# Performance work log

Measured on AMD Instinct MI355X. Metric: run time of the kernel, lower is better.

The kernel has to match this reference:

```python
import jax, jax.numpy as jnp
import numpy as np

D_MODEL, N_HEADS, D_HEAD = 1024, 16, 64
BATCH, SEQ = 4, 2048


def setup_inputs() -> dict:
    key = jax.random.key(0)
    ks = jax.random.split(key, 10)
    s = 1.0 / np.sqrt(D_MODEL)
    x = jax.random.normal(ks[0], (BATCH, SEQ, D_MODEL), dtype=jnp.float32)
    attention_mask = jax.random.randint(ks[1], (BATCH, SEQ), 0, 2).astype(jnp.bool_)
    # guarantee at least one attended key per batch row (avoid all -inf softmax)
    attention_mask = attention_mask.at[:, 0].set(True)
    def lin(k):
        kw, kb = jax.random.split(k)
        W = jax.random.uniform(kw, (D_MODEL, D_MODEL), jnp.float32, -s, s)
        b = jax.random.uniform(kb, (D_MODEL,), jnp.float32, -s, s)
        return W, b
    Wq, bq = lin(ks[2]); Wk, bk = lin(ks[3]); Wv, bv = lin(ks[4]); Wo, bo = lin(ks[5])
    return {"x": x, "attention_mask": attention_mask,
            "Wq": Wq, "bq": bq, "Wk": Wk, "bk": bk,
            "Wv": Wv, "bv": bv, "Wo": Wo, "bo": bo}


def reference(x, attention_mask, Wq, bq, Wk, bk, Wv, bv, Wo, bo):
    B, S, _ = x.shape
    def proj(W, b):  # [B,S,d_model] -> [B,S,H,Dh]
        return (x @ W + b).reshape(B, S, N_HEADS, D_HEAD)
    q = proj(Wq, bq)
    k = proj(Wk, bk)
    v = proj(Wv, bv)
    scores = jnp.einsum('bqhd,bkhd->bhqk', q, k)  # [B,H,S,S]
    add_mask = jnp.where(attention_mask, 0.0, jnp.inf)[:, None, None, :]
    # faithful order: subtract mask, THEN scale (inf survives division)
    probs = jax.nn.softmax((scores - add_mask) / jnp.sqrt(jnp.float32(D_HEAD)), axis=-1)
    attn = jnp.einsum('bhqk,bkhd->bqhd', probs, v).reshape(B, S, N_HEADS * D_HEAD)
    return attn @ Wo + bo
```

## Files before the change

kernel.cpp:

```cpp
#include <hip/hip_runtime.h>
#include <hip/hip_bf16.h>
#include <math.h>

#define BATCH 4
#define SEQ   2048
#define DM    1024
#define NH    16
#define DH    64
#define MROWS (BATCH * SEQ)

typedef unsigned short ushort_t;
typedef unsigned int   uint_t;
typedef __attribute__((ext_vector_type(8))) short  short8;
typedef __attribute__((ext_vector_type(4))) float  float4v;

#define QSCALE 0.1803368801111244f

__device__ __forceinline__ ushort_t f2bf(float v) {
    uint_t u = __float_as_uint(v);
    u += 0x7FFFu + ((u >> 16) & 1u);
    return (ushort_t)(u >> 16);
}
__device__ __forceinline__ float bf2f(ushort_t h) {
    return __uint_as_float(((uint_t)h) << 16);
}
__device__ __forceinline__ void gload_lds16(const ushort_t* g, ushort_t* lds) {
    __builtin_amdgcn_global_load_lds(
        (const __attribute__((address_space(1))) void*)g,
        (__attribute__((address_space(3))) void*)lds, 16, 0, 0);
}

__global__ __launch_bounds__(256) void conv_x(
    const float* __restrict__ src, ushort_t* __restrict__ dst, int n4)
{
    int i = blockIdx.x * 256 + threadIdx.x;
#pragma unroll
    for (int k = 0; k < 4; k++, i += 524288) {
        float4 v = ((const float4*)src)[i];
        ((ushort4*)dst)[i] = make_ushort4(f2bf(v.x), f2bf(v.y), f2bf(v.z), f2bf(v.w));
    }
}

__global__ __launch_bounds__(256) void convT_w4(
    const float* __restrict__ W0, const float* __restrict__ W1,
    const float* __restrict__ W2, const float* __restrict__ W3,
    ushort_t* __restrict__ fused, ushort_t* __restrict__ woh,
    ushort_t* __restrict__ wol)
{
    __shared__ float sT[64][65];
    const int z = blockIdx.z;
    const float* W = (z == 0) ? W0 : (z == 1) ? W1 : (z == 2) ? W2 : W3;
    ushort_t* ht = (z < 3) ? fused + (size_t)z * 1024 * 1024 : woh;
    const int n0 = blockIdx.x * 64, k0 = blockIdx.y * 64;
    const int t = threadIdx.x;
#pragma unroll
    for (int i = 0; i < 16; i++) {
        int idx = t + i * 256, r = idx >> 6, c = idx & 63;
        sT[r][c] = W[(size_t)(k0 + r) * 1024 + n0 + c];
    }
    __syncthreads();
#pragma unroll
    for (int i = 0; i < 16; i++) {
        int idx = t + i * 256, r = idx >> 6, c = idx & 63;
        float v = sT[c][r];
        ushort_t h = f2bf(v);
        ht[(size_t)(n0 + r) * 1024 + k0 + c] = h;
        if (z == 3) wol[(size_t)(n0 + r) * 1024 + k0 + c] = f2bf(v - bf2f(h));
    }
}

#define BAR()   asm volatile("s_barrier" ::: "memory")
#define LGKM0() asm volatile("s_waitcnt lgkmcnt(0)" ::: "memory")
#define VMW6()  asm volatile("s_waitcnt vmcnt(6)" ::: "memory")

#define STAGE_A(BO, KT) do {                                                 \
    const ushort_t* _s = prowA + (size_t)((KT) & 15) * 64;                   \
    gload_lds16(_s,         &smem[(BO) + dstw]);                             \
    gload_lds16(_s + 65536, &smem[(BO) + 4096 + dstw]);                      \
  } while (0)

#define STAGE_B(BO, KT) do {                                                 \
    const ushort_t* _s = prowB + (size_t)((KT) & 15) * 64;                   \
    gload_lds16(_s,          &smem[(BO) + 8192  + dstw]);                    \
    gload_lds16(_s + 65536,  &smem[(BO) + 12288 + dstw]);                    \
    gload_lds16(_s + 131072, &smem[(BO) + 16384 + dstw]);                    \
    gload_lds16(_s + 196608, &smem[(BO) + 20480 + dstw]);                    \
  } while (0)

#define LOAD_AV(BO) do {                                                     \
    _Pragma("unroll")                                                        \
    for (int mf = 0; mf < 4; mf++) {                                         \
      av[mf][0] = *(const short8*)&smem[(BO) + aAm + mf * 1024 + aA0];       \
      av[mf][1] = *(const short8*)&smem[(BO) + aAm + mf * 1024 + aA1];       \
    }                                                                        \
  } while (0)

#define LOAD_BV(BO, NQ) do {                                                 \
    _Pragma("unroll")                                                        \
    for (int nf = 0; nf < 2; nf++) {                                         \
      bvf[nf][0] = *(const short8*)&smem[(BO) + 8192 + aBn + (NQ) * 2048 +   \
                                         nf * 1024 + aA0];                   \
      bvf[nf][1] = *(const short8*)&smem[(BO) + 8192 + aBn + (NQ) * 2048 +   \
                                         nf * 1024 + aA1];                   \
    }                                                                        \
  } while (0)

#define MFMA_H(NQ) do {                                                      \
    __builtin_amdgcn_s_setprio(1);                                           \
    _Pragma("unroll")                                                        \
    for (int kk = 0; kk < 2; kk++)                                           \
      _Pragma("unroll")                                                      \
      for (int nf = 0; nf < 2; nf++)                                         \
        _Pragma("unroll")                                                    \
        for (int mf = 0; mf < 4; mf++)                                       \
          acc[mf][(NQ) * 2 + nf] =                                           \
              __builtin_amdgcn_mfma_f32_16x16x32_bf16(                       \
                  av[mf][kk], bvf[nf][kk], acc[mf][(NQ) * 2 + nf], 0, 0, 0); \
    __builtin_amdgcn_s_setprio(0);                                           \
  } while (0)

__global__ __launch_bounds__(512, 2) void gemm_qkv(
    const ushort_t* __restrict__ A, const ushort_t* __restrict__ Bt,
    const float* __restrict__ bq, const float* __restrict__ bk,
    const float* __restrict__ bv, const int* __restrict__ mask,
    ushort_t* __restrict__ Qh, ushort_t* __restrict__ Kh,
    ushort_t* __restrict__ Vt)
{
    __shared__ __align__(16) ushort_t smem[73728];
    const int t = threadIdx.x, lane = t & 63, w = t >> 6;

    int bid = blockIdx.y * 12 + blockIdx.x;
    bid = (bid & 7) * 96 + (bid >> 3);
    const int n0 = (bid % 12) * 256, m0 = (bid / 12) * 128;

    const int wm = w >> 2, wn = w & 3;
    const int lq = lane >> 4, lc = lane & 15;
    const int gl = (lane & 7) ^ ((lane >> 3) & 7);
    const int sect = n0 >> 10;
    const float* bsel = (sect == 0) ? bq : (sect == 1) ? bk : bv;
    const float scl = (sect == 0) ? QSCALE : 1.0f;

    const ushort_t* prowA = A  + (size_t)(m0 + w * 8 + (lane >> 3)) * 1024 + gl * 8;
    const ushort_t* prowB = Bt + (size_t)(n0 + w * 8 + (lane >> 3)) * 1024 + gl * 8;
    const int dstw = w * 512;

    const int aA0 = lc * 64 + ((lq ^ (lc & 7)) * 8);
    const int aA1 = lc * 64 + (((4 + lq) ^ (lc & 7)) * 8);
    const int aAm = wm * 4096;
    const int aBn = wn * 4096;

    float4v acc[4][4];
#pragma unroll
    for (int i = 0; i < 4; i++)
#pragma unroll
        for (int j = 0; j < 4; j++) acc[i][j] = (float4v)(0.0f);

    short8 av[4][2], bvf[2][2];

    STAGE_A(0, 0); STAGE_B(0, 0); STAGE_A(24576, 1); STAGE_B(24576, 1);
    VMW6();
    BAR();

    int bc = 0, bs = 49152;
    for (int kt = 0; kt < 16; kt++) {
        LOAD_AV(bc); LOAD_BV(bc, 0); STAGE_A(bs, kt + 2);
        BAR(); LGKM0(); MFMA_H(0); BAR();
        LOAD_BV(bc, 1); STAGE_B(bs, kt + 2);
        BAR(); LGKM0(); MFMA_H(1); VMW6(); BAR();
        bc = (bc == 49152) ? 0 : bc + 24576;
        bs = (bs == 49152) ? 0 : bs + 24576;
    }

#pragma unroll
    for (int nf = 0; nf < 4; nf++) {
        const int nn = (n0 + wn * 64 + nf * 16 + lc) & 1023;
        const float bvv = bsel[nn];
        const int h = nn >> 6, d = nn & 63;
#pragma unroll
        for (int mf = 0; mf < 4; mf++) {
            const int mbase = m0 + wm * 64 + mf * 16 + lq * 4;
            const int b = mbase >> 11, s0 = mbase & 2047;
            int mk[4] = {1, 1, 1, 1};
            if (sect != 0) {
                const int4 m4 = *(const int4*)&mask[b * 2048 + s0];
                mk[0] = m4.x; mk[1] = m4.y; mk[2] = m4.z; mk[3] = m4.w;
            }
            if (sect == 2) {
                ushort_t hh[4];
#pragma unroll
                for (int r = 0; r < 4; r++)
                    hh[r] = mk[r] ? f2bf(acc[mf][nf][r] + bvv) : (ushort_t)0;
                *(ushort4*)&Vt[((size_t)(b * 16 + h) * 64 + d) * 2048 + s0] =
                    make_ushort4(hh[0], hh[1], hh[2], hh[3]);
            } else {
                ushort_t* dst = (sect == 0) ? Qh : Kh;
#pragma unroll
                for (int r = 0; r < 4; r++)
                    dst[((size_t)(b * 16 + h) * 2048 + s0 + r) * 64 + d] =
                        mk[r] ? f2bf((acc[mf][nf][r] + bvv) * scl) : (ushort_t)0;
            }
        }
    }
}

#undef STAGE_A
#undef STAGE_B
#undef LOAD_AV
#undef LOAD_BV
#undef MFMA_H

#define S3_STAGE3A(BO, KT) do {                                              \
    const size_t _k = (size_t)((KT) & 31) * 32;                              \
    gload_lds16(pAh + _k, &smem[(BO) + toff]);                               \
    gload_lds16(pAl + _k, &smem[(BO) + 4096 + toff]);                        \
    gload_lds16(pBh + _k, &smem[(BO) + 8192 + toff]);                        \
  } while (0)

#define S3_STAGE3B(BO, KT) do {                                              \
    const size_t _k = (size_t)((KT) & 31) * 32;                              \
    gload_lds16(pBh + 131072 + _k, &smem[(BO) + 12288 + toff]);              \
    gload_lds16(pBl + _k,          &smem[(BO) + 16384 + toff]);              \
    gload_lds16(pBl + 131072 + _k, &smem[(BO) + 20480 + toff]);              \
  } while (0)

#define S3_MFMA(NQ) do {                                                     \
    __builtin_amdgcn_s_setprio(1);                                           \
    _Pragma("unroll")                                                        \
    for (int nf = 0; nf < 2; nf++)                                           \
      _Pragma("unroll")                                                      \
      for (int mf = 0; mf < 4; mf++) {                                       \
        float4v* _a = &acc[mf][(NQ) * 2 + nf];                               \
        *_a = __builtin_amdgcn_mfma_f32_16x16x32_bf16(ah[mf], bh[nf], *_a, 0, 0, 0); \
        *_a = __builtin_amdgcn_mfma_f32_16x16x32_bf16(al[mf], bh[nf], *_a, 0, 0, 0); \
        *_a = __builtin_amdgcn_mfma_f32_16x16x32_bf16(ah[mf], bl[nf], *_a, 0, 0, 0); \
      }                                                                      \
    __builtin_amdgcn_s_setprio(0);                                           \
  } while (0)

__global__ __launch_bounds__(512, 2) void gemm_split3(
    const ushort_t* __restrict__ Ah, const ushort_t* __restrict__ Al,
    const ushort_t* __restrict__ Bh, const ushort_t* __restrict__ Bl,
    const float* __restrict__ bias, float* __restrict__ out)
{
    __shared__ __align__(16) ushort_t smem[73728];
    const int t = threadIdx.x, lane = t & 63, w = t >> 6;

    int bid = blockIdx.y * 4 + blockIdx.x;
    bid = (bid & 7) * 32 + (bid >> 3);
    const int n0 = (bid % 4) * 256, m0 = (bid / 4) * 128;

    const int wm = w >> 2, wn = w & 3;
    const int lq = lane >> 4, lc = lane & 15;

    const int prow = t >> 2;
    const int pc = (t & 3) ^ (prow & 3);
    const size_t offA = (size_t)(m0 + prow) * 1024 + pc * 8;
    const size_t offB = (size_t)(n0 + prow) * 1024 + pc * 8;
    const ushort_t* pAh = Ah + offA;
    const ushort_t* pAl = Al + offA;
    const ushort_t* pBh = Bh + offB;
    const ushort_t* pBl = Bl + offB;
    const int toff = t * 8;

    const int aR = lc * 32 + ((lq ^ (lc & 3)) * 8);
    const int aAm = wm * 2048;
    const int aBn = wn * 2048;

    float4v acc[4][4];
#pragma unroll
    for (int i = 0; i < 4; i++)
#pragma unroll
        for (int j = 0; j < 4; j++) acc[i][j] = (float4v)(0.0f);

    short8 ah[4], al[4], bh[2], bl[2];

    S3_STAGE3A(0, 0);     S3_STAGE3B(0, 0);
    S3_STAGE3A(24576, 1); S3_STAGE3B(24576, 1);
    VMW6();
    BAR();

    int bc = 0, bs = 49152;
    for (int kt = 0; kt < 32; kt++) {
#pragma unroll
        for (int mf = 0; mf < 4; mf++) {
            ah[mf] = *(const short8*)&smem[bc + aAm + mf * 512 + aR];
            al[mf] = *(const short8*)&smem[bc + 4096 + aAm + mf * 512 + aR];
        }
#pragma unroll
        for (int nf = 0; nf < 2; nf++) {
            bh[nf] = *(const short8*)&smem[bc + 8192 + aBn + nf * 512 + aR];
            bl[nf] = *(const short8*)&smem[bc + 16384 + aBn + nf * 512 + aR];
        }
        S3_STAGE3A(bs, kt + 2);
        BAR(); LGKM0(); S3_MFMA(0); BAR();

#pragma unroll
        for (int nf = 0; nf < 2; nf++) {
            bh[nf] = *(const short8*)&smem[bc + 8192 + aBn + 1024 + nf * 512 + aR];
            bl[nf] = *(const short8*)&smem[bc + 16384 + aBn + 1024 + nf * 512 + aR];
        }
        S3_STAGE3B(bs, kt + 2);
        BAR(); LGKM0(); S3_MFMA(1); VMW6(); BAR();

        bc = (bc == 49152) ? 0 : bc + 24576;
        bs = (bs == 49152) ? 0 : bs + 24576;
    }

#pragma unroll
    for (int nf = 0; nf < 4; nf++) {
        const int n = n0 + wn * 64 + nf * 16 + lc;
        const float bvv = bias[n];
#pragma unroll
        for (int mf = 0; mf < 4; mf++)
#pragma unroll
            for (int r = 0; r < 4; r++) {
                const int m = m0 + wm * 64 + mf * 16 + lq * 4 + r;
                out[(size_t)m * 1024 + n] = acc[mf][nf][r] + bvv;
            }
    }
}

#undef S3_STAGE3A
#undef S3_STAGE3B
#undef S3_MFMA
#undef BAR
#undef LGKM0
#undef VMW6

#define FBAR()  asm volatile("s_barrier" ::: "memory")
#define FVMW4() asm volatile("s_waitcnt vmcnt(4)" ::: "memory")

__global__ __launch_bounds__(512, 2) void flash_mfma(
    const ushort_t* __restrict__ Q, const ushort_t* __restrict__ K,
    const ushort_t* __restrict__ Vt, const int* __restrict__ mask,
    ushort_t* __restrict__ Oh, ushort_t* __restrict__ Ol)
{
    __shared__ __align__(16) ushort_t smem[57344];
    const int t = threadIdx.x, lane = t & 63, w = t >> 6;

    const int i = blockIdx.y * 4 + blockIdx.x;
    const int bh = (i & 7) + ((i >> 5) << 3);
    const int q0 = ((i >> 3) & 3) * 512;
    const int b = bh >> 4, h = bh & 15;

    const int lq = lane >> 4, lc = lane & 15, lc7 = lc & 7;
    const int wq = w * 64;

    const int4 ma = ((const int4*)(mask + b * SEQ))[t];

    const int trow = lane >> 3;
    const int gl = (lane & 7) ^ (trow & 7);
    const ushort_t* qsrc = Q + ((size_t)bh * SEQ + q0 + wq + trow) * 64 + gl * 8;
#pragma unroll
    for (int j = 0; j < 8; j++)
        gload_lds16(qsrc + j * 512, &smem[w * 4096 + j * 512 + lane * 8]);

    const int strow = t >> 3;
    const int sgl = (t & 7) ^ (strow & 7);
    const ushort_t* kbase = K  + ((size_t)bh * SEQ + strow) * 64 + sgl * 8;
    const ushort_t* vbase = Vt + ((size_t)bh * 64 + strow) * SEQ + sgl * 8;
    gload_lds16(kbase,        &smem[32768 + t * 8]);
    gload_lds16(vbase,        &smem[45056 + t * 8]);
    gload_lds16(kbase + 4096, &smem[32768 + 4096 + t * 8]);
    gload_lds16(vbase + 64,   &smem[45056 + 4096 + t * 8]);

    int cnt = (ma.x == 0) + (ma.y == 0) + (ma.z == 0) + (ma.w == 0);
#pragma unroll
    for (int off = 1; off < 64; off <<= 1) cnt += __shfl_xor(cnt, off);
    if (lane == 0) ((float*)&smem[40960])[w] = (float)cnt;

    FBAR();

    const float* cs = (const float*)&smem[40960];
    const float nmaskf = cs[0] + cs[1] + cs[2] + cs[3] +
                         cs[4] + cs[5] + cs[6] + cs[7];

    FVMW4();
    short8 aq[4][2];
#pragma unroll
    for (int mt = 0; mt < 4; mt++)
#pragma unroll
        for (int kk = 0; kk < 2; kk++) {
            const int r = mt * 16 + lc;
            aq[mt][kk] = *(const short8*)&smem[w * 4096 + r * 64 +
                                               (((kk * 4 + lq) ^ (r & 7)) * 8)];
        }
    FBAR();

    int aK[2], aPw[4];
#pragma unroll
    for (int kk = 0; kk < 2; kk++)
        aK[kk] = lc * 64 + (((kk * 4 + lq) ^ lc7) * 8);
#pragma unroll
    for (int kt4 = 0; kt4 < 4; kt4++)
        aPw[kt4] = lc * 64 + (((kt4 * 2 + (lq >> 1)) ^ lc7) * 8) + (lq & 1) * 4;

    float4v O[4][4];
    float ladd[4];
#pragma unroll
    for (int mt = 0; mt < 4; mt++) {
#pragma unroll
        for (int nt = 0; nt < 4; nt++) O[mt][nt] = (float4v)(0.0f);
        ladd[mt] = 0.0f;
    }

    int cb = 0, sb = 2;
    for (int kt = 0; kt < 32; kt++) {
        const int kn = (kt + 2) & 31;
        gload_lds16(kbase + kn * 4096, &smem[32768 + sb * 4096 + t * 8]);
        gload_lds16(vbase + kn * 64,   &smem[45056 + sb * 4096 + t * 8]);
        FVMW4();
        FBAR();

        const int kb = 32768 + cb * 4096;
        const int vb = 45056 + cb * 4096;
        const int pb = w * 4096;

#pragma unroll
        for (int kt4 = 0; kt4 < 4; kt4++) {
            float4v sc[4];
#pragma unroll
            for (int mt = 0; mt < 4; mt++) sc[mt] = (float4v)(0.0f);
#pragma unroll
            for (int kk = 0; kk < 2; kk++) {
                const short8 ak = *(const short8*)&smem[kb + kt4 * 1024 + aK[kk]];
#pragma unroll
                for (int mt = 0; mt < 4; mt++)
                    sc[mt] = __builtin_amdgcn_mfma_f32_16x16x32_bf16(ak, aq[mt][kk], sc[mt], 0, 0, 0);
            }
#pragma unroll
            for (int mt = 0; mt < 4; mt++) {
                const float p0 = __builtin_amdgcn_exp2f(sc[mt][0]);
                const float p1 = __builtin_amdgcn_exp2f(sc[mt][1]);
                const float p2 = __builtin_amdgcn_exp2f(sc[mt][2]);
                const float p3 = __builtin_amdgcn_exp2f(sc[mt][3]);
                __hip_bfloat162 pk01 = __float22bfloat162_rn(make_float2(p0, p1));
                __hip_bfloat162 pk23 = __float22bfloat162_rn(make_float2(p2, p3));
                const uint_t u01 = *(const uint_t*)&pk01;
                const uint_t u23 = *(const uint_t*)&pk23;
                ladd[mt] += __uint_as_float(u01 << 16) + __uint_as_float(u01 & 0xffff0000u)
                          + __uint_as_float(u23 << 16) + __uint_as_float(u23 & 0xffff0000u);
                *(uint2*)&smem[pb + mt * 1024 + aPw[kt4]] = make_uint2(u01, u23);
            }
        }

#pragma unroll
        for (int kk = 0; kk < 2; kk++) {
            short8 ap[4];
#pragma unroll
            for (int mt = 0; mt < 4; mt++)
                ap[mt] = *(const short8*)&smem[pb + mt * 1024 + aK[kk]];
            __builtin_amdgcn_s_setprio(1);
#pragma unroll
            for (int nt = 0; nt < 4; nt++) {
                const short8 bv = *(const short8*)&smem[vb + nt * 1024 + aK[kk]];
#pragma unroll
                for (int mt = 0; mt < 4; mt++)
                    O[mt][nt] = __builtin_amdgcn_mfma_f32_16x16x32_bf16(ap[mt], bv, O[mt][nt], 0, 0, 0);
            }
            __builtin_amdgcn_s_setprio(0);
        }
        FBAR();

        cb = (cb == 2) ? 0 : cb + 1;
        sb = (sb == 2) ? 0 : sb + 1;
    }

    float lred[4];
#pragma unroll
    for (int mt = 0; mt < 4; mt++) {
        float v = ladd[mt];
        v += __shfl_xor(v, 16);
        v += __shfl_xor(v, 32);
        lred[mt] = v;
    }
    if (lq == 0) {
#pragma unroll
        for (int mt = 0; mt < 4; mt++)
            ((float*)smem)[w * 2048 + mt * 16 + lc] = lred[mt];
    }
    __syncthreads();

#pragma unroll
    for (int mt = 0; mt < 4; mt++) {
#pragma unroll
        for (int r = 0; r < 4; r++) {
            const float lsum =
                ((const float*)smem)[w * 2048 + mt * 16 + lq * 4 + r] - nmaskf;
            const float inv = 1.0f / lsum;
            const int srow = q0 + wq + mt * 16 + lq * 4 + r;
#pragma unroll
            for (int nt = 0; nt < 4; nt++) {
                const float v = O[mt][nt][r] * inv;
                const ushort_t hh = f2bf(v);
                const size_t idx = ((size_t)(b * SEQ + srow)) * 1024 + h * 64 + nt * 16 + lc;
                Oh[idx] = hh;
                Ol[idx] = f2bf(v - bf2f(hh));
            }
        }
    }
}

#undef FBAR
#undef FVMW4

extern "C" void kernel_launch(void* const* d_in, const int* in_sizes, int n_in,
                              void* d_out, int out_size, void* d_ws, size_t ws_size,
                              hipStream_t stream) {
    const float* x    = (const float*)d_in[0];
    const int*   mask = (const int*)d_in[1];
    const float* Wq   = (const float*)d_in[2];
    const float* bq   = (const float*)d_in[3];
    const float* Wk   = (const float*)d_in[4];
    const float* bk   = (const float*)d_in[5];
    const float* Wv   = (const float*)d_in[6];
    const float* bv   = (const float*)d_in[7];
    const float* Wo   = (const float*)d_in[8];
    const float* bo   = (const float*)d_in[9];
    float* out = (float*)d_out;

    ushort_t* p = (ushort_t*)d_ws;
    const size_t PLANE  = (size_t)MROWS * DM;
    const size_t WPLANE = (size_t)DM * DM;
    ushort_t* xh  = p;  p += PLANE;
    ushort_t* wf  = p;  p += 3 * WPLANE;
    ushort_t* woh = p;  p += WPLANE;
    ushort_t* wol = p;  p += WPLANE;
    ushort_t* Qh  = p;  p += PLANE;
    ushort_t* Kh  = p;  p += PLANE;
    ushort_t* Vth = p;  p += PLANE;
    ushort_t* Ath = p;  p += PLANE;
    ushort_t* Atl = p;  p += PLANE;

    dim3 blk(256);
    hipLaunchKernelGGL(conv_x, dim3(2048), blk, 0, stream, x, xh, 2097152);
    hipLaunchKernelGGL(convT_w4, dim3(16, 16, 4), blk, 0, stream,
                       Wq, Wk, Wv, Wo, wf, woh, wol);
    hipLaunchKernelGGL(gemm_qkv, dim3(12, 64), dim3(512), 0, stream,
                       xh, wf, bq, bk, bv, mask, Qh, Kh, Vth);
    hipLaunchKernelGGL(flash_mfma, dim3(4, 64), dim3(512), 0, stream,
                       Qh, Kh, Vth, mask, Ath, Atl);
    hipLaunchKernelGGL(gemm_split3, dim3(4, 64), dim3(512), 0, stream,
                       Ath, Atl, woh, wol, bo, out);
}
```

Measured before the change: 323.8 us.

## Shrink flash blocks to 256 threads, double-buffer K/V, compute row sums via MFMA

The flash attention kernel moves from 512-thread blocks covering 512 queries to 256-thread blocks covering 256 queries. Shared memory drops from 112 KB to 64 KB, and the triple-buffered K/V ring becomes a two-stage buffer that waits on vmcnt(0) at the end of each iteration. The softmax denominator is now accumulated by an extra MFMA against a ones vector instead of scalar bf16 unpack-adds, which removes the cross-wave reduction through shared memory. The aim is more resident blocks per CU and fewer VALU operations, at the cost of twice as many K/V loads across blocks and less prefetch depth.

```diff
diff --git a/kernel.cpp b/kernel.cpp
--- a/kernel.cpp
+++ b/kernel.cpp
@@ -327,94 +327,100 @@
 #undef LGKM0
 #undef VMW6
 
-#define FBAR()  asm volatile("s_barrier" ::: "memory")
-#define FVMW4() asm volatile("s_waitcnt vmcnt(4)" ::: "memory")
-
-__global__ __launch_bounds__(512, 2) void flash_mfma(
+#define FBAR()   asm volatile("s_barrier" ::: "memory")
+#define FLGKM0() asm volatile("s_waitcnt lgkmcnt(0)" ::: "memory")
+#define FVMW0()  asm volatile("s_waitcnt vmcnt(0)" ::: "memory")
+
+__global__ __launch_bounds__(256, 2) void flash_mfma(
     const ushort_t* __restrict__ Q, const ushort_t* __restrict__ K,
     const ushort_t* __restrict__ Vt, const int* __restrict__ mask,
     ushort_t* __restrict__ Oh, ushort_t* __restrict__ Ol)
 {
-    __shared__ __align__(16) ushort_t smem[57344];
+    __shared__ __align__(16) ushort_t smem[32768];
     const int t = threadIdx.x, lane = t & 63, w = t >> 6;
-
-    const int i = blockIdx.y * 4 + blockIdx.x;
-    const int bh = (i & 7) + ((i >> 5) << 3);
-    const int q0 = ((i >> 3) & 3) * 512;
-    const int b = bh >> 4, h = bh & 15;
-
-    const int lq = lane >> 4, lc = lane & 15, lc7 = lc & 7;
+    const int q0 = blockIdx.x * 256;
+    const int bh = blockIdx.y, b = bh >> 4, h = bh & 15;
+    const int lq = lane >> 4, lc = lane & 15;
+    const int lcs = (lc & 7) ^ ((lc >> 3) << 2);
     const int wq = w * 64;
 
-    const int4 ma = ((const int4*)(mask + b * SEQ))[t];
+    const short8 onesf = (short8)(lc == 0 ? (short)0x3F80 : (short)0);
+
+    const int4 ma0 = ((const int4*)(mask + b * SEQ))[t];
+    const int4 ma1 = ((const int4*)(mask + b * SEQ))[t + 256];
 
     const int trow = lane >> 3;
-    const int gl = (lane & 7) ^ (trow & 7);
-    const ushort_t* qsrc = Q + ((size_t)bh * SEQ + q0 + wq + trow) * 64 + gl * 8;
-#pragma unroll
-    for (int j = 0; j < 8; j++)
-        gload_lds16(qsrc + j * 512, &smem[w * 4096 + j * 512 + lane * 8]);
-
-    const int strow = t >> 3;
-    const int sgl = (t & 7) ^ (strow & 7);
-    const ushort_t* kbase = K  + ((size_t)bh * SEQ + strow) * 64 + sgl * 8;
-    const ushort_t* vbase = Vt + ((size_t)bh * 64 + strow) * SEQ + sgl * 8;
-    gload_lds16(kbase,        &smem[32768 + t * 8]);
-    gload_lds16(vbase,        &smem[45056 + t * 8]);
-    gload_lds16(kbase + 4096, &smem[32768 + 4096 + t * 8]);
-    gload_lds16(vbase + 64,   &smem[45056 + 4096 + t * 8]);
-
-    int cnt = (ma.x == 0) + (ma.y == 0) + (ma.z == 0) + (ma.w == 0);
+    const int gl0 = (lane & 7) ^ trow;
+    const ushort_t* qbase = Q + ((size_t)bh * SEQ + q0 + wq + trow) * 64;
+    const ushort_t* qE = qbase + gl0 * 8;
+    const ushort_t* qO = qbase + 512 + (gl0 ^ 4) * 8;
+#pragma unroll
+    for (int j = 0; j < 4; j++) {
+        gload_lds16(qE + j * 1024, &smem[w * 4096 + (2 * j) * 512 + lane * 8]);
+        gload_lds16(qO + j * 1024, &smem[w * 4096 + (2 * j + 1) * 512 + lane * 8]);
+    }
+
+    const int sgl = (t & 7) ^ ((t >> 3) & 7) ^ (((t >> 6) & 1) << 2);
+    const ushort_t* kb0 = K  + ((size_t)bh * SEQ + (t >> 3)) * 64 + sgl * 8;
+    const ushort_t* vb0 = Vt + ((size_t)bh * 64 + (t >> 3)) * SEQ + sgl * 8;
+
+    gload_lds16(kb0,             &smem[16384 + t * 8]);
+    gload_lds16(kb0 + 2048,      &smem[16384 + 2048 + t * 8]);
+    gload_lds16(vb0,             &smem[24576 + t * 8]);
+    gload_lds16(vb0 + 32 * SEQ,  &smem[24576 + 2048 + t * 8]);
+
+    int cnt = (ma0.x == 0) + (ma0.y == 0) + (ma0.z == 0) + (ma0.w == 0) +
+              (ma1.x == 0) + (ma1.y == 0) + (ma1.z == 0) + (ma1.w == 0);
 #pragma unroll
     for (int off = 1; off < 64; off <<= 1) cnt += __shfl_xor(cnt, off);
-    if (lane == 0) ((float*)&smem[40960])[w] = (float)cnt;
-
+    if (lane == 0) ((float*)&smem[28672])[w] = (float)cnt;
+
+    __syncthreads();
+
+    const float* cs = (const float*)&smem[28672];
+    const float nmaskf = cs[0] + cs[1] + cs[2] + cs[3];
+
+    int aKo[2], aPw[4];
+#pragma unroll
+    for (int kk = 0; kk < 2; kk++)
+        aKo[kk] = lc * 64 + (((kk * 4 + lq) ^ lcs) * 8);
+#pragma unroll
+    for (int kt4 = 0; kt4 < 4; kt4++)
+        aPw[kt4] = lc * 64 + (((kt4 * 2 + (lq >> 1)) ^ lcs) * 8) + (lq & 1) * 4;
+
+    short8 aq[4][2];
+#pragma unroll
+    for (int mt = 0; mt < 4; mt++)
+#pragma unroll
+        for (int kk = 0; kk < 2; kk++)
+            aq[mt][kk] = *(const short8*)&smem[w * 4096 + mt * 1024 + aKo[kk]];
+
+    FLGKM0();
     FBAR();
 
-    const float* cs = (const float*)&smem[40960];
-    const float nmaskf = cs[0] + cs[1] + cs[2] + cs[3] +
-                         cs[4] + cs[5] + cs[6] + cs[7];
-
-    FVMW4();
-    short8 aq[4][2];
-#pragma unroll
-    for (int mt = 0; mt < 4; mt++)
-#pragma unroll
-        for (int kk = 0; kk < 2; kk++) {
-            const int r = mt * 16 + lc;
-            aq[mt][kk] = *(const short8*)&smem[w * 4096 + r * 64 +
-                                               (((kk * 4 + lq) ^ (r & 7)) * 8)];
-        }
-    FBAR();
-
-    int aK[2], aPw[4];
-#pragma unroll
-    for (int kk = 0; kk < 2; kk++)
-        aK[kk] = lc * 64 + (((kk * 4 + lq) ^ lc7) * 8);
-#pragma unroll
-    for (int kt4 = 0; kt4 < 4; kt4++)
-        aPw[kt4] = lc * 64 + (((kt4 * 2 + (lq >> 1)) ^ lc7) * 8) + (lq & 1) * 4;
-
     float4v O[4][4];
-    float ladd[4];
+    float4v lacc[4];
 #pragma unroll
     for (int mt = 0; mt < 4; mt++) {
 #pragma unroll
         for (int nt = 0; nt < 4; nt++) O[mt][nt] = (float4v)(0.0f);
-        ladd[mt] = 0.0f;
-    }
-
-    int cb = 0, sb = 2;
+        lacc[mt] = (float4v)(0.0f);
+    }
+
     for (int kt = 0; kt < 32; kt++) {
-        const int kn = (kt + 2) & 31;
-        gload_lds16(kbase + kn * 4096, &smem[32768 + sb * 4096 + t * 8]);
-        gload_lds16(vbase + kn * 64,   &smem[45056 + sb * 4096 + t * 8]);
-        FVMW4();
-        FBAR();
-
-        const int kb = 32768 + cb * 4096;
-        const int vb = 45056 + cb * 4096;
-        const int pb = w * 4096;
+        const int cur = (kt & 1) * 4096;
+        const int nxt = cur ^ 4096;
+
+        if (kt < 31) {
+            const ushort_t* kn = kb0 + (size_t)(kt + 1) * 4096;
+            const ushort_t* vn = vb0 + (size_t)(kt + 1) * 64;
+            gload_lds16(kn,            &smem[16384 + nxt + t * 8]);
+            gload_lds16(kn + 2048,     &smem[16384 + nxt + 2048 + t * 8]);
+            gload_lds16(vn,            &smem[24576 + nxt + t * 8]);
+            gload_lds16(vn + 32 * SEQ, &smem[24576 + nxt + 2048 + t * 8]);
+        }
+
+        const int kb = 16384 + cur, vb = 24576 + cur, pb = w * 4096;
 
 #pragma unroll
         for (int kt4 = 0; kt4 < 4; kt4++) {
@@ -423,7 +429,7 @@
             for (int mt = 0; mt < 4; mt++) sc[mt] = (float4v)(0.0f);
 #pragma unroll
             for (int kk = 0; kk < 2; kk++) {
-                const short8 ak = *(const short8*)&smem[kb + kt4 * 1024 + aK[kk]];
+                const short8 ak = *(const short8*)&smem[kb + kt4 * 1024 + aKo[kk]];
 #pragma unroll
                 for (int mt = 0; mt < 4; mt++)
                     sc[mt] = __builtin_amdgcn_mfma_f32_16x16x32_bf16(ak, aq[mt][kk], sc[mt], 0, 0, 0);
@@ -436,11 +442,8 @@
                 const float p3 = __builtin_amdgcn_exp2f(sc[mt][3]);
                 __hip_bfloat162 pk01 = __float22bfloat162_rn(make_float2(p0, p1));
                 __hip_bfloat162 pk23 = __float22bfloat162_rn(make_float2(p2, p3));
-                const uint_t u01 = *(const uint_t*)&pk01;
-                const uint_t u23 = *(const uint_t*)&pk23;
-                ladd[mt] += __uint_as_float(u01 << 16) + __uint_as_float(u01 & 0xffff0000u)
-                          + __uint_as_float(u23 << 16) + __uint_as_float(u23 & 0xffff0000u);
-                *(uint2*)&smem[pb + mt * 1024 + aPw[kt4]] = make_uint2(u01, u23);
+                *(uint2*)&smem[pb + mt * 1024 + aPw[kt4]] =
+                    make_uint2(*(const uint_t*)&pk01, *(const uint_t*)&pk23);
             }
         }
 
@@ -449,44 +452,30 @@
             short8 ap[4];
 #pragma unroll
             for (int mt = 0; mt < 4; mt++)
-                ap[mt] = *(const short8*)&smem[pb + mt * 1024 + aK[kk]];
+                ap[mt] = *(const short8*)&smem[pb + mt * 1024 + aKo[kk]];
             __builtin_amdgcn_s_setprio(1);
 #pragma unroll
+            for (int mt = 0; mt < 4; mt++)
+                lacc[mt] = __builtin_amdgcn_mfma_f32_16x16x32_bf16(ap[mt], onesf, lacc[mt], 0, 0, 0);
+#pragma unroll
             for (int nt = 0; nt < 4; nt++) {
-                const short8 bv = *(const short8*)&smem[vb + nt * 1024 + aK[kk]];
+                const short8 bv = *(const short8*)&smem[vb + nt * 1024 + aKo[kk]];
 #pragma unroll
                 for (int mt = 0; mt < 4; mt++)
                     O[mt][nt] = __builtin_amdgcn_mfma_f32_16x16x32_bf16(ap[mt], bv, O[mt][nt], 0, 0, 0);
             }
             __builtin_amdgcn_s_setprio(0);
         }
+
+        FVMW0();
         FBAR();
-
-        cb = (cb == 2) ? 0 : cb + 1;
-        sb = (sb == 2) ? 0 : sb + 1;
-    }
-
-    float lred[4];
+    }
+
 #pragma unroll
     for (int mt = 0; mt < 4; mt++) {
-        float v = ladd[mt];
-        v += __shfl_xor(v, 16);
-        v += __shfl_xor(v, 32);
-        lred[mt] = v;
-    }
-    if (lq == 0) {
-#pragma unroll
-        for (int mt = 0; mt < 4; mt++)
-            ((float*)smem)[w * 2048 + mt * 16 + lc] = lred[mt];
-    }
-    __syncthreads();
-
-#pragma unroll
-    for (int mt = 0; mt < 4; mt++) {
 #pragma unroll
         for (int r = 0; r < 4; r++) {
-            const float lsum =
-                ((const float*)smem)[w * 2048 + mt * 16 + lq * 4 + r] - nmaskf;
+            const float lsum = __shfl(lacc[mt][r], lane & 48) - nmaskf;
             const float inv = 1.0f / lsum;
             const int srow = q0 + wq + mt * 16 + lq * 4 + r;
 #pragma unroll
@@ -502,7 +491,8 @@
 }
 
 #undef FBAR
-#undef FVMW4
+#undef FLGKM0
+#undef FVMW0
 
 extern "C" void kernel_launch(void* const* d_in, const int* in_sizes, int n_in,
                               void* d_out, int out_size, void* d_ws, size_t ws_size,
@@ -538,7 +528,7 @@
                        Wq, Wk, Wv, Wo, wf, woh, wol);
     hipLaunchKernelGGL(gemm_qkv, dim3(12, 64), dim3(512), 0, stream,
                        xh, wf, bq, bk, bv, mask, Qh, Kh, Vth);
-    hipLaunchKernelGGL(flash_mfma, dim3(4, 64), dim3(512), 0, stream,
+    hipLaunchKernelGGL(flash_mfma, dim3(8, 64), blk, 0, stream,
                        Qh, Kh, Vth, mask, Ath, Atl);
     hipLaunchKernelGGL(gemm_split3, dim3(4, 64), dim3(512), 0, stream,
                        Ath, Atl, woh, wol, bo, out);
```

Result: no change. 324.9 us (+0.3%).
